# Optimization experiments

Hardware: AMD Instinct MI355X
Metric: run time of the kernel (lower is better)

The kernel has to match this reference:

```python
import jax, jax.numpy as jnp
import numpy as np

K = 32
MAX_ITER = 30
STOP_COND = 1e-07
TIE_EPS = 1e-08


def _all_dist(C, X):
    # squared Euclidean distance matrix: (B, N, K)
    xx = jnp.sum(X * X, axis=-1)[:, :, None]      # (B, N, 1)
    cc = jnp.sum(C * C, axis=-1)[:, None, :]      # (B, 1, K)
    xc = jnp.einsum('bnd,bkd->bnk', X, C)         # (B, N, K)
    return cc + xx - 2.0 * xc


def setup_inputs() -> dict:
    key = jax.random.key(0)
    k1, k2 = jax.random.split(key)
    E = jax.random.normal(k1, (4, 8192, 64), dtype=jnp.float32)
    log_W = jax.random.normal(k2, (4, 8192), dtype=jnp.float32)
    return {"E": E, "log_W": log_W}


def reference(E, log_W):
    B, N, D = E.shape
    key = jax.random.key(42)
    k_init, k_loop = jax.random.split(key)

    # sel_vectors: random K distinct points as initial centroids
    sel = jax.random.permutation(k_init, N)[:K]
    C0 = E[:, sel, :]                              # (B, K, D)
    ass0 = jnp.zeros((B, N, K), dtype=E.dtype)
    done0 = jnp.array(False)

    def step(carry, it):
        C, ass, X, done = carry
        Dm = _all_dist(C, X)                       # (B, N, K)
        mind = jnp.min(Dm, axis=2)                 # (B, N)
        ass_new = (jnp.abs(Dm - mind[:, :, None]) < TIE_EPS).astype(X.dtype)
        df = jnp.sum(jnp.abs(ass_new - ass), axis=(1, 2)) / N   # (B,)
        done_now = done | jnp.all(df < STOP_COND)

        # soft weighting over members of each cluster (exp of log_W, masked)
        aw = ass_new * log_W[:, :, None] - 100.0 * (1.0 - ass_new)
        aw = aw - jnp.max(aw, axis=1, keepdims=True)
        aw = jnp.exp(aw) * ass_new                 # (B, N, K)
        ass_fat = jnp.sum(aw, axis=1, keepdims=True)   # (B, 1, K)
        ass_norm = aw / jnp.clip(ass_fat, 1e-12, None)

        # empty-cluster handling: replace data rows at empty-cluster indices
        # with random data points (mirrors in-place X mutation in torch code)
        kk = jax.random.fold_in(k_loop, it)
        repl_idx = jax.random.randint(kk, (X.shape[0], K), 0, N)
        repl = jnp.take_along_axis(X, repl_idx[:, :, None], axis=1)  # (B, K, D)
        empty = (ass_fat[:, 0, :] == 0)[:, :, None]                  # (B, K, 1)
        X_new = X.at[:, :K, :].set(jnp.where(empty, repl, X[:, :K, :]))

        C_new = jnp.einsum('bnk,bnd->bkd', ass_norm, X_new)

        # freeze state once converged (torch breaks before updating ass/C)
        C = jnp.where(done_now, C, C_new)
        ass = jnp.where(done_now, ass, ass_new)
        X = jnp.where(done_now, X, X_new)
        return (C, ass, X, done_now), None

    (C, ass, X, _), _ = jax.lax.scan(step, (C0, ass0, E, done0), jnp.arange(MAX_ITER))

    # final stats
    Dm = _all_dist(C, X)
    mind = jnp.min(Dm, axis=2)                     # (B, N)
    obj = jnp.mean(mind, axis=1)                   # (B,)
    mind_rep = jnp.min(Dm, axis=1)                 # (B, K)
    rep_idx = jnp.argmin(Dm, axis=1)               # (B, K)
    ass_rep = (jnp.abs(Dm - mind_rep[:, None, :]) < TIE_EPS).astype(X.dtype)
    ass_rep = ass_rep / jnp.clip(jnp.sum(ass_rep, axis=1, keepdims=True), 0.001, None)
    rep = jnp.einsum('bnk,bnd->bkd', ass_rep, X)   # (B, K, D)

    return ass, C, rep, rep_idx, obj
```

## Files before the change

### kernel.cpp

```cpp
#include <hip/hip_runtime.h>
#include <stdint.h>

typedef unsigned int u32;
typedef unsigned long long u64;

#define Bb 4
#define Nn 8192
#define Dd 64
#define Kk 32
#define MAXIT 30
#define NBLK 256
#define RPB  64
#define NTH  512

#define ACC_STRIDE 2112

enum : u32 {
  WS_BAR   = 0u,
  WS_MASKH = 192u,
  WS_TBAR  = 1280u,
  WS_XHEAD = 34048u,
  WS_KEYS1 = 66816u,
  WS_KEYS2 = 99584u,
  WS_A1    = 132352u,
  WS_A2    = 197888u,
  WS_ACC   = 263424u,
  WS_CHG   = 364800u,
  WS_POBJ  = 364864u,
  WS_PMIN  = 365888u,
  WS_DM    = 431424u,
  WS_HIST1 = 4625728u,
  WS_HIST2 = 4658496u
};

__device__ __forceinline__ void tf2x32(u32 k0, u32 k1, u32 x0, u32 x1, u32& o0, u32& o1){
  u32 ks2 = k0 ^ k1 ^ 0x1BD11BDAu;
  x0 += k0; x1 += k1;
#define TFR(r) { x0 += x1; x1 = (x1<<(r))|(x1>>(32-(r))); x1 ^= x0; }
  TFR(13) TFR(15) TFR(26) TFR(6)
  x0 += k1;  x1 += ks2 + 1u;
  TFR(17) TFR(29) TFR(16) TFR(24)
  x0 += ks2; x1 += k0 + 2u;
  TFR(13) TFR(15) TFR(26) TFR(6)
  x0 += k0;  x1 += k1 + 3u;
  TFR(17) TFR(29) TFR(16) TFR(24)
  x0 += k1;  x1 += ks2 + 4u;
  TFR(13) TFR(15) TFR(26) TFR(6)
  x0 += ks2; x1 += k0 + 5u;
#undef TFR
  o0 = x0; o1 = x1;
}

__global__ __launch_bounds__(1024, 1) void kzero(char* __restrict__ ws){
  const int tid = threadIdx.x;
  u32* bar   = (u32*)(ws + WS_BAR);
  u32* tbar  = (u32*)(ws + WS_TBAR);
  float* CHG = (float*)(ws + WS_CHG);
  float* ACC0 = (float*)(ws + WS_ACC);
  u32* h1 = (u32*)(ws + WS_HIST1);
  u32* h2 = (u32*)(ws + WS_HIST2);
  if (tid < 4) bar[tid] = 0u;
  if (tid < 96) tbar[tid] = 0u;
  if (tid < 3) CHG[tid] = 0.f;
  for (int i = tid; i < Bb*ACC_STRIDE; i += 1024) ACC0[i] = 0.f;
  for (int i = tid; i < 8192; i += 1024){ h1[i] = 0u; h2[i] = 0u; }
}

__device__ __forceinline__ void grid_barrier(char* ws, int b){
  __syncthreads();
  if (threadIdx.x == 0){
    u32* root = (u32*)(ws + WS_TBAR);
    u32* flag = (u32*)(ws + WS_TBAR + 64);
    u32* leaf = (u32*)(ws + WS_TBAR + 128 + (size_t)b*64);
    u32 g = __hip_atomic_load(flag, __ATOMIC_RELAXED, __HIP_MEMORY_SCOPE_AGENT);
    bool waiter = true;
    u32 a = __hip_atomic_fetch_add(leaf, 1u, __ATOMIC_ACQ_REL, __HIP_MEMORY_SCOPE_AGENT);
    if (a == (u32)(RPB-1)){
      u32 ra = __hip_atomic_fetch_add(root, 1u, __ATOMIC_ACQ_REL, __HIP_MEMORY_SCOPE_AGENT);
      if (ra == (u32)(Bb-1)){
        __hip_atomic_store(root, 0u, __ATOMIC_RELAXED, __HIP_MEMORY_SCOPE_AGENT);
        #pragma unroll
        for (int i = 0; i < Bb; i++)
          __hip_atomic_store((u32*)(ws + WS_TBAR + 128 + (size_t)i*64), 0u,
                             __ATOMIC_RELAXED, __HIP_MEMORY_SCOPE_AGENT);
        __hip_atomic_store(flag, g + 1u, __ATOMIC_RELEASE, __HIP_MEMORY_SCOPE_AGENT);
        waiter = false;
      }
    }
    if (waiter){
      int polls = 0;
      for (;;){
        u32 v = __hip_atomic_load(flag, __ATOMIC_RELAXED, __HIP_MEMORY_SCOPE_AGENT);
        if (v != g) break;
        if ((++polls & 63) == 0){
          v = __hip_atomic_load(flag, __ATOMIC_ACQUIRE, __HIP_MEMORY_SCOPE_AGENT);
          if (v != g) break;
        }
        __builtin_amdgcn_s_sleep(2);
      }
    }
    __builtin_amdgcn_fence(__ATOMIC_ACQUIRE, "agent");
  }
  __syncthreads();
}

#define CALC_XXH() do { float s0=0.f,s1=0.f,s2=0.f,s3=0.f; \
  _Pragma("unroll") \
  for (int j=0;j<4;j++){ s0+=x[4*j]*x[4*j]; s1+=x[4*j+1]*x[4*j+1]; s2+=x[4*j+2]*x[4*j+2]; s3+=x[4*j+3]*x[4*j+3]; } \
  xxh=(s0+s1)+(s2+s3); } while(0)

#define CALC_DIST() do { \
  float xxf = xxh + __shfl_xor(xxh, 1); \
  xxf += __shfl_xor(xxf, 2); \
  _Pragma("unroll") \
  for (int k=0;k<32;k++){ \
    const float4* cp = (const float4*)&Cl[k*64 + h*16]; \
    float s0=0.f,s1=0.f,s2=0.f,s3=0.f; \
    _Pragma("unroll") \
    for (int j=0;j<4;j++){ float4 c = cp[j]; s0+=x[4*j]*c.x; s1+=x[4*j+1]*c.y; s2+=x[4*j+2]*c.z; s3+=x[4*j+3]*c.w; } \
    float dot=(s0+s1)+(s2+s3); \
    dot += __shfl_xor(dot, 1); \
    dot += __shfl_xor(dot, 2); \
    dloc[k]=(ccl[k]+xxf)-2.f*dot; \
  } } while(0)

__global__ __launch_bounds__(512, 1) void kmain(const float* __restrict__ E, const float* __restrict__ LW,
                                                float* __restrict__ out, char* __restrict__ ws){
  const int tid = threadIdx.x;
  const int bid = blockIdx.x;
  const int b   = bid >> 6;
  const int r   = bid & 63;
  const int h   = tid & 3;
  const int pl  = tid >> 2;
  const int n   = (r << 7) + pl;

  u32*   maskh = (u32*)(ws + WS_MASKH);
  float* XH    = (float*)(ws + WS_XHEAD);
  u32*   keys1 = (u32*)(ws + WS_KEYS1);
  u32*   keys2 = (u32*)(ws + WS_KEYS2);
  u64*   a1    = (u64*)(ws + WS_A1);
  u64*   a2    = (u64*)(ws + WS_A2);
  u32*   hist1 = (u32*)(ws + WS_HIST1);
  u32*   hist2 = (u32*)(ws + WS_HIST2);
  float* ACC   = (float*)(ws + WS_ACC);
  float* CHG   = (float*)(ws + WS_CHG);
  float* Pobj  = (float*)(ws + WS_POBJ);
  u64*   Pmin  = (u64*)(ws + WS_PMIN);
  float* Dm    = (float*)(ws + WS_DM);

  __shared__ float Cl[2048];
  __shared__ float ccl[32];
  __shared__ float part[ACC_STRIDE];
  __shared__ float newX[2048];
  __shared__ u64   kminl[32];
  __shared__ float red[512];
  __shared__ u32   scan[512];
  __shared__ u32   sel_s[32];
  __shared__ u32   sh_empty, sh_idx, sh_tcnt;
  __shared__ float sh_chgf, sh_mind;

  float x[16]; float xxh;
  { const float4* xr = (const float4*)(E + (size_t)(b*Nn + n)*Dd + h*16);
    #pragma unroll
    for (int j=0;j<4;j++){ float4 v = xr[j]; x[4*j]=v.x; x[4*j+1]=v.y; x[4*j+2]=v.z; x[4*j+3]=v.w; } }
  CALC_XXH();
  const float w = expf(LW[b*Nn + n]);

  {
    const int g = bid*NTH + tid;
    if (g < 8192){
      u32 i0,i1; tf2x32(0u,42u, 0u,0u, i0,i1);
      u32 key10,key11, s10,s11;
      tf2x32(i0,i1, 0u,0u, key10,key11);
      tf2x32(i0,i1, 0u,1u, s10,s11);
      u32 s20,s21; tf2x32(key10,key11, 0u,1u, s20,s21);
      u32 y0,y1;
      tf2x32(s10,s11, 0u,(u32)g, y0,y1); u32 k1x = y0 ^ y1;
      tf2x32(s20,s21, 0u,(u32)g, y0,y1); u32 k2x = y0 ^ y1;
      keys1[g] = k1x; keys2[g] = k2x;
      atomicAdd(&hist1[k1x>>19], 1u);
      atomicAdd(&hist2[k2x>>19], 1u);
      XH[g] = E[(size_t)(g>>11)*Nn*Dd + (size_t)(g & 2047)];
    }
  }
  grid_barrier(ws, b);
  if (bid < 2){
    u32* hh = bid ? hist2 : hist1;
    u32 loc[16]; u32 s = 0;
    #pragma unroll
    for (int j = 0; j < 16; j++){ loc[j] = hh[tid*16 + j]; s += loc[j]; }
    scan[tid] = s;
    __syncthreads();
    for (int st = 1; st < 512; st <<= 1){
      u32 v = (tid >= st) ? scan[tid - st] : 0u;
      __syncthreads();
      scan[tid] += v;
      __syncthreads();
    }
    u32 run = tid ? scan[tid-1] : 0u;
    #pragma unroll
    for (int j = 0; j < 16; j++){ u32 c = loc[j]; hh[tid*16 + j] = run; run += c; }
  }
  grid_barrier(ws, b);
  {
    const int g = bid*NTH + tid;
    if (g < 8192){
      u32 kx = keys1[g];
      u32 pos = atomicAdd(&hist1[kx>>19], 1u);
      a1[pos] = ((u64)kx << 32) | (u32)g;
      kx = keys2[g];
      pos = atomicAdd(&hist2[kx>>19], 1u);
      a2[pos] = ((u64)kx << 32) | (u32)g;
    }
  }
  grid_barrier(ws, b);
  if (tid < 64){
    int g2 = bid*32 + (tid & 31);
    u64* aa = (tid < 32) ? a1 : a2;
    u32* hh = (tid < 32) ? hist1 : hist2;
    int s0 = g2 ? (int)hh[g2-1] : 0;
    int e0 = (int)hh[g2];
    int m = e0 - s0;
    if (m > 1){
      if (m <= 16){
        u64 tv[16];
        #pragma unroll
        for (int j = 0; j < 16; j++) tv[j] = (j < m) ? aa[s0+j] : ~0ull;
        u64* sc = ((u64*)newX) + (size_t)tid*16;
        #pragma unroll
        for (int j = 0; j < 16; j++){ if (j < m) sc[j] = tv[j]; }
        for (int i2 = 1; i2 < m; i2++){
          u64 kx = sc[i2]; int j = i2-1;
          while (j >= 0 && sc[j] > kx){ sc[j+1] = sc[j]; j--; }
          sc[j+1] = kx;
        }
        #pragma unroll
        for (int j = 0; j < 16; j++){ if (j < m) aa[s0+j] = sc[j]; }
      } else {
        for (int i2 = s0+1; i2 < e0; i2++){
          u64 kx = aa[i2]; int j = i2-1;
          while (j >= s0 && aa[j] > kx){ aa[j+1] = aa[j]; j--; }
          aa[j+1] = kx;
        }
      }
    }
  }
  grid_barrier(ws, b);
  if (tid < 32){ u32 p = (u32)a2[tid]; sel_s[tid] = (u32)a1[p]; }
  __syncthreads();
  for (int i = tid; i < 2048; i += NTH){
    Cl[i] = E[(size_t)b*Nn*Dd + (size_t)sel_s[i>>6]*Dd + (i & 63)];
  }

  u32 kl0, kl1; tf2x32(0u,42u, 0u,1u, kl0, kl1);

  __syncthreads();
  if (tid < 32){ float s=0.f; const float* cr=&Cl[tid*64];
    #pragma unroll
    for (int d2=0; d2<64; d2++) s += cr[d2]*cr[d2];
    ccl[tid]=s; }
  __syncthreads();

  u32 prevmask = 0u;
  float dloc[32];

  for (int it = 0; it < MAXIT; it++){
    const int par = it & 1;
    const int cur = it % 3, nxt = (it + 1) % 3;
    CALC_DIST();
    float mind = dloc[0];
    #pragma unroll
    for (int k=1;k<32;k++) mind = fminf(mind, dloc[k]);
    u32 mask = 0u;
    #pragma unroll
    for (int k=0;k<32;k++) if (fabsf(dloc[k]-mind) < 1e-8f) mask |= (1u<<k);
    int changed = (h==0) ? ((it==0) ? 1 : (mask != prevmask)) : 0;
    prevmask = mask;
    if (r == 0 && tid < 128 && h == 0) maskh[par*128 + b*32 + pl] = mask;

    __syncthreads();
    for (int i = tid; i < ACC_STRIDE; i += 512) part[i] = 0.f;
    __syncthreads();
    { u32 mm = mask;
      while (mm){
        int k = __ffs(mm) - 1; mm &= mm - 1;
        #pragma unroll
        for (int d2=0; d2<16; d2++) atomicAdd(&part[(h*16 + d2)*32 + k], w*x[d2]);
        if (h == 0){
          atomicAdd(&part[2048 + k], w);
          atomicAdd(&part[2080 + k], 1.0f);
        }
      } }
    int nchg = __syncthreads_count(changed);
    { float* dst = ACC + (size_t)cur*Bb*ACC_STRIDE + b*ACC_STRIDE;
      for (int i = tid; i < ACC_STRIDE; i += 512) unsafeAtomicAdd(&dst[i], part[i]);
      if (tid == 0 && nchg) unsafeAtomicAdd(&CHG[cur], (float)nchg);
      float* nz = ACC + (size_t)nxt*Bb*ACC_STRIDE + b*ACC_STRIDE;
      if (tid < 33) nz[r*33 + tid] = 0.f;
      if (b == 0 && r == 0 && tid == 33) CHG[nxt] = 0.f;
    }
    grid_barrier(ws, b);

    { const float* src = ACC + (size_t)cur*Bb*ACC_STRIDE;
      for (int i = tid; i < ACC_STRIDE; i += 512) part[i] = src[b*ACC_STRIDE + i];
      float cv = 1.f;
      if (tid < 128) cv = src[(tid >> 5)*ACC_STRIDE + 2080 + (tid & 31)];
      if (tid == 0) sh_chgf = CHG[cur];
      int anyempty = __syncthreads_or(cv == 0.f);
      if (sh_chgf == 0.f) break;

      { bool e = (tid < 32) && (part[2080 + tid] == 0.f);
        u64 bal = __ballot(e);
        if (tid == 0) sh_empty = (u32)bal; }
      __syncthreads();
      u32 em = sh_empty;

      if (anyempty){
        u32 g0, g1; tf2x32(kl0, kl1, 0u, (u32)it, g0, g1);
        for (int k = 0; k < 32; k++){
          if (!((em >> k) & 1u)) continue;
          int j = b*32 + k;
          u32 y0, y1; tf2x32(g0, g1, 0u, (u32)j, y0, y1);
          u32 ridx = (y0 ^ y1) & 8191u;
          u32 mj = maskh[par*128 + b*32 + k];
          float wj = expf(LW[b*Nn + k]);
          if (tid < 64){
            float xo = XH[(b*32 + k)*64 + tid];
            float xn = (ridx < 32u) ? XH[(b*32 + (int)ridx)*64 + tid]
                                    : E[(size_t)(b*Nn + (int)ridx)*Dd + tid];
            newX[k*64 + tid] = xn;
            float dxw = wj * (xn - xo);
            u32 m2 = mj;
            while (m2){ int kq = __ffs(m2) - 1; m2 &= m2 - 1; part[tid*32 + kq] += dxw; }
          }
        }
        __syncthreads();
        grid_barrier(ws, b);
        if (r == 0){
          for (int k = 0; k < 32; k++){
            if (!((em >> k) & 1u)) continue;
            if (tid < 64) XH[(b*32 + k)*64 + tid] = newX[k*64 + tid];
          }
          __syncthreads();
          if (tid < 128 && ((em >> pl) & 1u)){
            #pragma unroll
            for (int d2 = 0; d2 < 16; d2++) x[d2] = newX[pl*64 + h*16 + d2];
            CALC_XXH();
          }
        }
      }
    }
    __syncthreads();
    for (int i = tid; i < 2048; i += 512){
      int k = i >> 6, d = i & 63;
      Cl[i] = part[d*32 + k] / fmaxf(part[2048 + k], 1e-12f);
    }
    __syncthreads();
    if (tid < 32){ float s=0.f; const float* cr=&Cl[tid*64];
      #pragma unroll
      for (int d2=0; d2<64; d2++) s += cr[d2]*cr[d2];
      ccl[tid]=s; }
    __syncthreads();
  }

  CALC_DIST();
  float mind = dloc[0];
  #pragma unroll
  for (int k=1;k<32;k++) mind = fminf(mind, dloc[k]);
  #pragma unroll
  for (int kq=0;kq<8;kq++){
    int k = h*8 + kq;
    Dm[(size_t)(b*32 + k)*Nn + n] = dloc[k];
  }
  { float4* dst = (float4*)(out + (size_t)(b*Nn + n)*32);
    #pragma unroll
    for (int qq=0;qq<2;qq++){
      int q = h*2 + qq;
      float4 v;
      v.x = ((prevmask>>(4*q  ))&1u) ? 1.f : 0.f;
      v.y = ((prevmask>>(4*q+1))&1u) ? 1.f : 0.f;
      v.z = ((prevmask>>(4*q+2))&1u) ? 1.f : 0.f;
      v.w = ((prevmask>>(4*q+3))&1u) ? 1.f : 0.f;
      dst[q] = v;
    } }
  if (tid < 32) kminl[tid] = ~0ull;
  red[tid] = (h==0) ? mind : 0.f;
  __syncthreads();
  #pragma unroll
  for (int kq=0;kq<8;kq++){
    int k = h*8 + kq;
    u32 u = __float_as_uint(dloc[k]);
    u = (u & 0x80000000u) ? ~u : (u | 0x80000000u);
    u64 pk = ((u64)u << 32) | (u32)n;
    atomicMin(&kminl[k], pk);
  }
  for (int s2 = 256; s2 > 0; s2 >>= 1){
    if (tid < s2) red[tid] += red[tid + s2];
    __syncthreads();
  }
  if (tid < 32) Pmin[(size_t)(b*32 + tid)*64 + r] = kminl[tid];
  if (tid == 0) Pobj[b*64 + r] = red[0];
  grid_barrier(ws, b);

  if (bid < 128){
    const int b2 = bid >> 5, k2 = bid & 31;
    const size_t OFF_C    = (size_t)Bb*Nn*Kk;
    const size_t OFF_REP  = OFF_C + (size_t)Bb*Kk*Dd;
    const size_t OFF_RIDX = OFF_REP + (size_t)Bb*Kk*Dd;
    const size_t OFF_OBJ  = OFF_RIDX + (size_t)Bb*Kk;
    if (tid == 0){
      u64 m = ~0ull;
      for (int bl = 0; bl < 64; bl++){ u64 v = Pmin[(size_t)(b2*32 + k2)*64 + bl]; if (v < m) m = v; }
      u32 enc = (u32)(m >> 32);
      u32 ub  = (enc & 0x80000000u) ? (enc & 0x7fffffffu) : ~enc;
      sh_mind = __uint_as_float(ub);
      sh_idx  = (u32)(m & 0xffffffffu);
      sh_tcnt = 0u;
    }
    if (tid < 64) newX[tid] = 0.f;
    __syncthreads();
    float mr = sh_mind;
    for (int nn = tid; nn < Nn; nn += 512){
      float dv = Dm[(size_t)(b2*32 + k2)*Nn + nn];
      if (fabsf(dv - mr) < 1e-8f){
        atomicAdd(&sh_tcnt, 1u);
        const float* xr = (nn < 32) ? &XH[(b2*32 + nn)*64] : &E[(size_t)(b2*Nn + nn)*Dd];
        for (int d2 = 0; d2 < 64; d2++) atomicAdd(&newX[d2], xr[d2]);
      }
    }
    __syncthreads();
    if (tid < 64){
      out[OFF_C   + (size_t)(b2*32 + k2)*64 + tid] = Cl[k2*64 + tid];
      out[OFF_REP + (size_t)(b2*32 + k2)*64 + tid] = newX[tid] / (float)sh_tcnt;
    }
    if (tid == 0) out[OFF_RIDX + b2*32 + k2] = (float)sh_idx;
    if (k2 == 0){
      if (tid < 64) red[tid] = Pobj[b2*64 + tid];
      __syncthreads();
      if (tid == 0){ float s = 0.f; for (int i2 = 0; i2 < 64; i2++) s += red[i2];
        out[OFF_OBJ + b2] = s / (float)Nn; }
    }
  }
}

extern "C" void kernel_launch(void* const* d_in, const int* in_sizes, int n_in,
                              void* d_out, int out_size, void* d_ws, size_t ws_size,
                              hipStream_t stream) {
  const float* E  = (const float*)d_in[0];
  const float* LW = (const float*)d_in[1];
  float* out = (float*)d_out;
  char*  ws  = (char*)d_ws;
  (void)in_sizes; (void)n_in; (void)out_size; (void)ws_size;
  kzero<<<dim3(1),    dim3(1024), 0, stream>>>(ws);
  kmain<<<dim3(NBLK), dim3(512),  0, stream>>>(E, LW, out, ws);
}
```

Before: 1.058 ms.

## Replace global atomic accumulation with per-block partials and distributed tree reduction

```diff
diff --git a/kernel.cpp b/kernel.cpp
--- a/kernel.cpp
+++ b/kernel.cpp
@@ -29,6 +29,7 @@
   WS_POBJ  = 364864u,
   WS_PMIN  = 365888u,
   WS_DM    = 431424u,
+  WS_PSUM  = 431424u,
   WS_HIST1 = 4625728u,
   WS_HIST2 = 4658496u
 };
@@ -56,13 +57,11 @@
   u32* bar   = (u32*)(ws + WS_BAR);
   u32* tbar  = (u32*)(ws + WS_TBAR);
   float* CHG = (float*)(ws + WS_CHG);
-  float* ACC0 = (float*)(ws + WS_ACC);
   u32* h1 = (u32*)(ws + WS_HIST1);
   u32* h2 = (u32*)(ws + WS_HIST2);
   if (tid < 4) bar[tid] = 0u;
   if (tid < 96) tbar[tid] = 0u;
   if (tid < 3) CHG[tid] = 0.f;
-  for (int i = tid; i < Bb*ACC_STRIDE; i += 1024) ACC0[i] = 0.f;
   for (int i = tid; i < 8192; i += 1024){ h1[i] = 0u; h2[i] = 0u; }
 }
 
@@ -143,6 +142,7 @@
   u32*   hist1 = (u32*)(ws + WS_HIST1);
   u32*   hist2 = (u32*)(ws + WS_HIST2);
   float* ACC   = (float*)(ws + WS_ACC);
+  float* PSUM  = (float*)(ws + WS_PSUM);
   float* CHG   = (float*)(ws + WS_CHG);
   float* Pobj  = (float*)(ws + WS_POBJ);
   u64*   Pmin  = (u64*)(ws + WS_PMIN);
@@ -150,7 +150,7 @@
 
   __shared__ float Cl[2048];
   __shared__ float ccl[32];
-  __shared__ float part[ACC_STRIDE];
+  __shared__ __align__(16) float part[ACC_STRIDE];
   __shared__ float newX[2048];
   __shared__ u64   kminl[32];
   __shared__ float red[512];
@@ -292,22 +292,38 @@
         }
       } }
     int nchg = __syncthreads_count(changed);
-    { float* dst = ACC + (size_t)cur*Bb*ACC_STRIDE + b*ACC_STRIDE;
-      for (int i = tid; i < ACC_STRIDE; i += 512) unsafeAtomicAdd(&dst[i], part[i]);
+    { float4* dst4 = (float4*)(PSUM + (size_t)(b*64 + r)*ACC_STRIDE);
+      const float4* p4 = (const float4*)part;
+      dst4[tid] = p4[tid];
+      if (tid < 16) dst4[512 + tid] = p4[512 + tid];
       if (tid == 0 && nchg) unsafeAtomicAdd(&CHG[cur], (float)nchg);
-      float* nz = ACC + (size_t)nxt*Bb*ACC_STRIDE + b*ACC_STRIDE;
-      if (tid < 33) nz[r*33 + tid] = 0.f;
       if (b == 0 && r == 0 && tid == 33) CHG[nxt] = 0.f;
     }
     grid_barrier(ws, b);
 
-    { const float* src = ACC + (size_t)cur*Bb*ACC_STRIDE;
-      for (int i = tid; i < ACC_STRIDE; i += 512) part[i] = src[b*ACC_STRIDE + i];
+    if (tid == 0) sh_chgf = CHG[cur];
+    __syncthreads();
+    if (sh_chgf == 0.f) break;
+
+    { const int wid = tid >> 6, lane = tid & 63;
+      const float* pb = PSUM + (size_t)(b*64 + lane)*ACC_STRIDE;
+      for (int e = wid; e < 33; e += 8){
+        int idx = r*33 + e;
+        float v = pb[idx];
+        v += __shfl_xor(v, 1);  v += __shfl_xor(v, 2);
+        v += __shfl_xor(v, 4);  v += __shfl_xor(v, 8);
+        v += __shfl_xor(v, 16); v += __shfl_xor(v, 32);
+        if (lane == 0) ACC[(size_t)b*ACC_STRIDE + idx] = v;
+      } }
+    grid_barrier(ws, b);
+
+    { const float4* s4 = (const float4*)(ACC + (size_t)b*ACC_STRIDE);
+      float4* p4 = (float4*)part;
+      p4[tid] = s4[tid];
+      if (tid < 16) p4[512 + tid] = s4[512 + tid];
       float cv = 1.f;
-      if (tid < 128) cv = src[(tid >> 5)*ACC_STRIDE + 2080 + (tid & 31)];
-      if (tid == 0) sh_chgf = CHG[cur];
+      if (tid < 128) cv = ACC[(size_t)(tid >> 5)*ACC_STRIDE + 2080 + (tid & 31)];
       int anyempty = __syncthreads_or(cv == 0.f);
-      if (sh_chgf == 0.f) break;
 
       { bool e = (tid < 32) && (part[2080 + tid] == 0.f);
         u64 bal = __ballot(e);
```

After: 1.484 ms. +40.3%, slower.
